# Kernel optimization log

Measured on AMD Instinct MI355X. Metric: run time of the kernel, lower is better.

The kernel has to match this reference:

```python
import jax, jax.numpy as jnp
import numpy as np
import math

EPS_LN = 1e-5
EPS_Q = 1e-5


def _layernorm(x):
    # LayerNorm without affine (elementwise_affine=False), biased variance
    mu = jnp.mean(x, axis=-1, keepdims=True)
    var = jnp.var(x, axis=-1, keepdims=True)
    return (x - mu) * jax.lax.rsqrt(var + EPS_LN)


def _quantize_activations(x):
    # per-row 8-bit absmax quantization
    eta = jnp.maximum(jnp.max(jnp.abs(x), axis=-1, keepdims=True), EPS_Q)
    x_q = jnp.clip(jnp.round(x * (127.0 / eta)), -128.0, 127.0)
    return x_q, eta / 127.0


def _quantize_weights(w):
    # absmean ternary quantization
    gamma = jnp.maximum(jnp.mean(jnp.abs(w)), EPS_Q)
    w_q = jnp.round(jnp.clip(w / gamma, -1.0, 1.0))
    return w_q, gamma


def setup_inputs() -> dict:
    key = jax.random.key(0)
    k1, k2 = jax.random.split(key, 2)
    B, S, IN, OUT = 2, 4096, 2048, 8192
    x = jax.random.normal(k1, (B, S, IN), dtype=jnp.float32)
    # kaiming_uniform_(a=sqrt(5)) -> U(-1/sqrt(fan_in), 1/sqrt(fan_in))
    bound = 1.0 / math.sqrt(IN)
    weight = jax.random.uniform(k2, (OUT, IN), dtype=jnp.float32, minval=-bound, maxval=bound)
    bias = jnp.zeros((OUT,), dtype=jnp.float32)
    return {"x": x, "weight": weight, "bias": bias}


def reference(x, weight, bias):
    x_norm = _layernorm(x)
    x_q, x_scale = _quantize_activations(x_norm)      # [B,S,K], [B,S,1]
    w_q, w_scale = _quantize_weights(weight)           # [N,K], scalar
    # int8 GEMM emulated exactly in fp32 (values are small integers, exact)
    out_i = jnp.einsum('bsk,nk->bsn', x_q, w_q)        # int32-equivalent accum
    out = out_i * (w_scale * x_scale) + bias
    return out
```

## Files before the change

kernel.cpp:

```cpp
#include <hip/hip_runtime.h>
#include <stdint.h>

typedef int v4i __attribute__((ext_vector_type(4)));

#define M_DIM 8192
#define N_DIM 8192
#define K_DIM 2048
#define RISKY_TAU 1e-4f
#define BUCKET_CAP 1024
#define SLOT 32768

#define ASYNC16(g, l) __builtin_amdgcn_global_load_lds(                        \
    (const __attribute__((address_space(1))) void*)(uintptr_t)(g),             \
    (__attribute__((address_space(3))) void*)(uint32_t)(uintptr_t)(l), 16, 0, 0)

__global__ __launch_bounds__(256) void abssum_stage1(const float* __restrict__ w,
                                                     float* __restrict__ s1) {
  int b = blockIdx.x * 256 + threadIdx.x;
  const float* p = w + (size_t)b * 128;
  float r[8];
#pragma unroll
  for (int j = 0; j < 8; j++) r[j] = fabsf(p[j]);
  for (int i = 8; i < 128; i += 8) {
#pragma unroll
    for (int j = 0; j < 8; j++) r[j] += fabsf(p[i + j]);
  }
  s1[b] = ((r[0] + r[1]) + (r[2] + r[3])) + ((r[4] + r[5]) + (r[6] + r[7]));
}

__global__ __launch_bounds__(256) void abssum_stage2(const float* __restrict__ s1,
                                                     float* __restrict__ s2) {
  int t = blockIdx.x * 256 + threadIdx.x;
  float v[32];
#pragma unroll
  for (int i = 0; i < 32; i++) v[i] = s1[t * 32 + i];
#pragma unroll
  for (int s = 1; s < 32; s *= 2) {
#pragma unroll
    for (int i = 0; i < 32; i += 2 * s) v[i] += v[i + s];
  }
  s2[t] = v[0];
}

__global__ __launch_bounds__(256) void gamma_stage3(const float* __restrict__ s2,
                                                    float* __restrict__ gp) {
  int t = threadIdx.x;
  float v[16];
#pragma unroll
  for (int i = 0; i < 16; i++) v[i] = s2[t * 16 + i];
#pragma unroll
  for (int s = 1; s < 16; s *= 2) {
#pragma unroll
    for (int i = 0; i < 16; i += 2 * s) v[i] += v[i + s];
  }
  __shared__ float sm[256];
  sm[t] = v[0];
  for (int s = 1; s < 256; s *= 2) {
    __syncthreads();
    if ((t & (2 * s - 1)) == 0) sm[t] += sm[t + s];
  }
  __syncthreads();
  if (t == 0) {
    float g = sm[0] * 0x1p-24f;
    gp[0] = fmaxf(g, 1e-5f);
  }
}

__global__ void zero_counts(int* __restrict__ counts) {
  counts[threadIdx.x] = 0;
}

__global__ __launch_bounds__(256) void wq_kernel(const float4* __restrict__ w4,
                                                 const float* __restrict__ gp,
                                                 int* __restrict__ wq,
                                                 int* __restrict__ counts,
                                                 int* __restrict__ buckets) {
  int i = blockIdx.x * 256 + threadIdx.x;
  float g = gp[0];
  float4 v = w4[i];
  float e[4] = {v.x, v.y, v.z, v.w};
  int q[4];
#pragma unroll
  for (int c = 0; c < 4; c++) {
    q[c] = (int)rintf(fminf(fmaxf(e[c] / g, -1.0f), 1.0f));
    float t = fabsf(e[c]) / g;
    if (fabsf(t - 0.5f) < RISKY_TAU) {
      int flat = i * 4 + c;
      int n = flat >> 11;
      int k = flat & 2047;
      int sgn_neg = (e[c] < 0.0f) ? 1 : 0;
      int sbit = (q[c] == 0) ? sgn_neg : (1 - sgn_neg);
      int b = n >> 7;
      int idx = atomicAdd(&counts[b], 1);
      if (idx < BUCKET_CAP)
        buckets[b * BUCKET_CAP + idx] = k | (n << 11) | (sbit << 24);
    }
  }
  wq[i] = (q[0] & 0xFF) | ((q[1] & 0xFF) << 8) | ((q[2] & 0xFF) << 16) | ((q[3] & 0xFF) << 24);
}

__global__ __launch_bounds__(256) void lnq_kernel(const float* __restrict__ x,
                                                  const float* __restrict__ gp,
                                                  int8_t* __restrict__ xq,
                                                  float* __restrict__ scales) {
  const int row = blockIdx.x;
  const int t = threadIdx.x;
  const float4* xr = (const float4*)(x + (size_t)row * K_DIM);
  float4 a = xr[t];
  float4 b = xr[t + 256];
  double v[8] = {a.x, a.y, a.z, a.w, b.x, b.y, b.z, b.w};
  double s = 0.0, ss = 0.0;
#pragma unroll
  for (int i = 0; i < 8; i++) { s += v[i]; ss += v[i] * v[i]; }
  __shared__ double sm1[256], sm2[256];
  sm1[t] = s; sm2[t] = ss;
  __syncthreads();
  for (int off = 128; off > 0; off >>= 1) {
    if (t < off) { sm1[t] += sm1[t + off]; sm2[t] += sm2[t + off]; }
    __syncthreads();
  }
  double mu = sm1[0] * (1.0 / 2048.0);
  double var = sm2[0] * (1.0 / 2048.0) - mu * mu;
  double inv = 1.0 / sqrt(var + 1e-5);
  __syncthreads();
  double mx = 0.0;
#pragma unroll
  for (int i = 0; i < 8; i++) {
    v[i] = (v[i] - mu) * inv;
    double av = fabs(v[i]);
    if (av > mx) mx = av;
  }
  sm1[t] = mx;
  __syncthreads();
  for (int off = 128; off > 0; off >>= 1) {
    if (t < off) sm1[t] = fmax(sm1[t], sm1[t + off]);
    __syncthreads();
  }
  double eta = fmax(sm1[0], 1e-5);
  double r = 127.0 / eta;
  int q[8];
#pragma unroll
  for (int i = 0; i < 8; i++) {
    double qq = rint(v[i] * r);
    qq = fmin(fmax(qq, -128.0), 127.0);
    q[i] = (int)qq;
  }
  int p0 = (q[0] & 0xFF) | ((q[1] & 0xFF) << 8) | ((q[2] & 0xFF) << 16) | ((q[3] & 0xFF) << 24);
  int p1 = (q[4] & 0xFF) | ((q[5] & 0xFF) << 8) | ((q[6] & 0xFF) << 16) | ((q[7] & 0xFF) << 24);
  int* orow = (int*)(xq + (size_t)row * K_DIM);
  orow[t] = p0;
  orow[t + 256] = p1;
  if (t == 0) scales[row] = (float)((double)gp[0] * eta * (1.0 / 127.0));
}

__global__ __launch_bounds__(512) void gemm_i8_kernel(const int8_t* __restrict__ A,
                                                      const int8_t* __restrict__ B,
                                                      const float* __restrict__ scales,
                                                      const float* __restrict__ bias,
                                                      const int* __restrict__ counts,
                                                      const int* __restrict__ buckets,
                                                      float* __restrict__ C) {
  __shared__ alignas(16) int8_t lds[3 * SLOT];
  const int tid = threadIdx.x;
  const int wave = tid >> 6;
  const int lane = tid & 63;

  const int b = blockIdx.x;
  const int tr = (b & 7) * 4 + ((b >> 3) & 3);
  const int tc = b >> 5;
  const int brow = tr * 256;
  const int bcol = tc * 256;

  const int chunkr = lane >> 2;
  const int sl = lane & 3;
  const int8_t* gA[2];
  const int8_t* gB[2];
  int dA[2], dB[2];
#pragma unroll
  for (int c = 0; c < 2; c++) {
    int ch = wave * 2 + c;
    int r = ch * 16 + chunkr;
    int scol = ((sl ^ ((r >> 1) & 3)) << 4);
    gA[c] = A + (size_t)(brow + r) * K_DIM + scol;
    gB[c] = B + (size_t)(bcol + r) * K_DIM + scol;
    dA[c] = ch * 1024;
    dB[c] = 16384 + ch * 1024;
  }

  const int wr = wave >> 2;
  const int wc = wave & 3;
  const int ks = lane >> 4;
  int aoff[8], boff[4];
#pragma unroll
  for (int m = 0; m < 8; m++) {
    int r = wr * 128 + m * 16 + (lane & 15);
    aoff[m] = r * 64 + ((ks ^ ((r >> 1) & 3)) << 4);
  }
#pragma unroll
  for (int n = 0; n < 4; n++) {
    int r = wc * 64 + n * 16 + (lane & 15);
    boff[n] = 16384 + r * 64 + ((ks ^ ((r >> 1) & 3)) << 4);
  }

  v4i acc[8][4];
  const v4i vzero = {0, 0, 0, 0};
#pragma unroll
  for (int m = 0; m < 8; m++)
#pragma unroll
    for (int n = 0; n < 4; n++) acc[m][n] = vzero;

#pragma unroll
  for (int c = 0; c < 2; c++) {
    ASYNC16(gA[c], lds + dA[c]);
    ASYNC16(gB[c], lds + dB[c]);
  }
#pragma unroll
  for (int c = 0; c < 2; c++) {
    ASYNC16(gA[c] + 64, lds + SLOT + dA[c]);
    ASYNC16(gB[c] + 64, lds + SLOT + dB[c]);
  }

  int rbase = 0;
  int sbase = 2 * SLOT;
  for (int t = 0; t < 32; ++t) {
    if (t < 31) asm volatile("s_waitcnt vmcnt(4)" ::: "memory");
    else        asm volatile("s_waitcnt vmcnt(0)" ::: "memory");
    __builtin_amdgcn_s_barrier();
    if (t < 30) {
      const int kt = (t + 2) * 64;
#pragma unroll
      for (int c = 0; c < 2; c++) {
        ASYNC16(gA[c] + kt, lds + sbase + dA[c]);
        ASYNC16(gB[c] + kt, lds + sbase + dB[c]);
      }
    }
    v4i bf[4], af[8];
#pragma unroll
    for (int n = 0; n < 4; n++) bf[n] = *(const v4i*)(lds + rbase + boff[n]);
#pragma unroll
    for (int m = 0; m < 8; m++) af[m] = *(const v4i*)(lds + rbase + aoff[m]);
    __builtin_amdgcn_s_setprio(1);
#pragma unroll
    for (int m = 0; m < 8; m++)
#pragma unroll
      for (int n = 0; n < 4; n++)
        acc[m][n] = __builtin_amdgcn_mfma_i32_16x16x64_i8(af[m], bf[n], acc[m][n], 0, 0, 0);
    __builtin_amdgcn_s_setprio(0);
    rbase = (rbase == 2 * SLOT) ? 0 : rbase + SLOT;
    sbase = (sbase == 2 * SLOT) ? 0 : sbase + SLOT;
  }

#pragma unroll
  for (int m = 0; m < 8; m++)
#pragma unroll
    for (int n = 0; n < 4; n++) acc[m][n] = acc[m][n] + acc[m][n];

  const int crow0 = brow + wr * 128;
  const int ccol0 = bcol + wc * 64;

#define CORR(J)                                                                \
  {                                                                            \
    _Pragma("unroll") for (int m = 0; m < 8; m++) {                            \
      _Pragma("unroll") for (int r = 0; r < 4; r++) {                          \
        int grow = crow0 + m * 16 + ((lane >> 4) << 2) + r;                    \
        int xv = (int)A[(size_t)grow * K_DIM + k];                             \
        acc[m][J][r] += sv * xv;                                               \
      }                                                                        \
    }                                                                          \
  }

  {
    int bkt = (bcol + wc * 64) >> 7;
    int cnt = counts[bkt];
    if (cnt > BUCKET_CAP) cnt = BUCKET_CAP;
    const int* bk = buckets + bkt * BUCKET_CAP;
    for (int e = 0; e < cnt; ++e) {
      int word = bk[e];
      int k = word & 2047;
      int nc = (word >> 11) & 8191;
      int sv = ((word >> 24) & 1) ? -1 : 1;
      if (((nc >> 6) & 1) == (wc & 1) && (nc & 15) == (lane & 15)) {
        int j = (nc >> 4) & 3;
        switch (j) {
          case 0: CORR(0); break;
          case 1: CORR(1); break;
          case 2: CORR(2); break;
          case 3: CORR(3); break;
        }
      }
    }
  }
#undef CORR

#pragma unroll
  for (int m = 0; m < 8; m++) {
#pragma unroll
    for (int r = 0; r < 4; r++) {
      int grow = crow0 + m * 16 + ((lane >> 4) << 2) + r;
      float sc = scales[grow] * 0.5f;
      float* crow = C + (size_t)grow * N_DIM;
#pragma unroll
      for (int n = 0; n < 4; n++) {
        int gcol = ccol0 + n * 16 + (lane & 15);
        crow[gcol] = (float)acc[m][n][r] * sc + bias[gcol];
      }
    }
  }
}

extern "C" void kernel_launch(void* const* d_in, const int* in_sizes, int n_in,
                              void* d_out, int out_size, void* d_ws, size_t ws_size,
                              hipStream_t stream) {
  const float* x = (const float*)d_in[0];
  const float* w = (const float*)d_in[1];
  const float* bias = (const float*)d_in[2];
  float* out = (float*)d_out;

  char* ws = (char*)d_ws;
  float* s1 = (float*)(ws);
  float* s2 = (float*)(ws + 0x100000);
  float* gamma_f = (float*)(ws + 0x110000);
  float* scales = (float*)(ws + 0x120000);
  int* counts = (int*)(ws + 0x130000);
  int* buckets = (int*)(ws + 0x131000);
  int8_t* Aq = (int8_t*)(ws + 0x200000);
  int8_t* Wq = (int8_t*)(ws + 0x200000 + (size_t)M_DIM * K_DIM);

  abssum_stage1<<<512, 256, 0, stream>>>(w, s1);
  abssum_stage2<<<16, 256, 0, stream>>>(s1, s2);
  gamma_stage3<<<1, 256, 0, stream>>>(s2, gamma_f);
  zero_counts<<<1, 64, 0, stream>>>(counts);
  wq_kernel<<<(N_DIM * K_DIM / 4 + 255) / 256, 256, 0, stream>>>(
      (const float4*)w, gamma_f, (int*)Wq, counts, buckets);
  lnq_kernel<<<M_DIM, 256, 0, stream>>>(x, gamma_f, Aq, scales);
  gemm_i8_kernel<<<1024, 512, 0, stream>>>(Aq, Wq, scales, bias, counts, buckets, out);
}
```

Measured before the change: 280.2 us.

## Interleave LDS reads and async global loads across four MFMA phases per K-tile

Measured after the change: 293.5 us. 4.7% more time.

```diff
diff --git a/kernel.cpp b/kernel.cpp
--- a/kernel.cpp
+++ b/kernel.cpp
@@ -219,36 +219,67 @@
     ASYNC16(gA[c] + 64, lds + SLOT + dA[c]);
     ASYNC16(gB[c] + 64, lds + SLOT + dB[c]);
   }
+  asm volatile("s_waitcnt vmcnt(4)" ::: "memory");
+  __builtin_amdgcn_s_barrier();
+
+#define MFMA2(M)                                                               \
+  _Pragma("unroll") for (int n = 0; n < 4; n++)                                \
+    acc[M][n] = __builtin_amdgcn_mfma_i32_16x16x64_i8(af[M], bf[n], acc[M][n], 0, 0, 0); \
+  _Pragma("unroll") for (int n = 0; n < 4; n++)                                \
+    acc[M + 1][n] = __builtin_amdgcn_mfma_i32_16x16x64_i8(af[M + 1], bf[n], acc[M + 1][n], 0, 0, 0);
 
   int rbase = 0;
   int sbase = 2 * SLOT;
   for (int t = 0; t < 32; ++t) {
-    if (t < 31) asm volatile("s_waitcnt vmcnt(4)" ::: "memory");
-    else        asm volatile("s_waitcnt vmcnt(0)" ::: "memory");
-    __builtin_amdgcn_s_barrier();
-    if (t < 30) {
-      const int kt = (t + 2) * 64;
-#pragma unroll
-      for (int c = 0; c < 2; c++) {
-        ASYNC16(gA[c] + kt, lds + sbase + dA[c]);
-        ASYNC16(gB[c] + kt, lds + sbase + dB[c]);
-      }
-    }
+    const int kt = (t + 2) * 64;
+    const bool st = (t < 30);
     v4i bf[4], af[8];
-#pragma unroll
-    for (int n = 0; n < 4; n++) bf[n] = *(const v4i*)(lds + rbase + boff[n]);
-#pragma unroll
-    for (int m = 0; m < 8; m++) af[m] = *(const v4i*)(lds + rbase + aoff[m]);
+    bf[0] = *(const v4i*)(lds + rbase + boff[0]);
+    bf[1] = *(const v4i*)(lds + rbase + boff[1]);
+    bf[2] = *(const v4i*)(lds + rbase + boff[2]);
+    bf[3] = *(const v4i*)(lds + rbase + boff[3]);
+    af[0] = *(const v4i*)(lds + rbase + aoff[0]);
+    af[1] = *(const v4i*)(lds + rbase + aoff[1]);
+    if (st) ASYNC16(gA[0] + kt, lds + sbase + dA[0]);
+    __builtin_amdgcn_s_barrier();
     __builtin_amdgcn_s_setprio(1);
-#pragma unroll
-    for (int m = 0; m < 8; m++)
-#pragma unroll
-      for (int n = 0; n < 4; n++)
-        acc[m][n] = __builtin_amdgcn_mfma_i32_16x16x64_i8(af[m], bf[n], acc[m][n], 0, 0, 0);
+    MFMA2(0)
     __builtin_amdgcn_s_setprio(0);
+    __builtin_amdgcn_s_barrier();
+    asm volatile("" ::: "memory");
+    af[2] = *(const v4i*)(lds + rbase + aoff[2]);
+    af[3] = *(const v4i*)(lds + rbase + aoff[3]);
+    if (st) ASYNC16(gA[1] + kt, lds + sbase + dA[1]);
+    __builtin_amdgcn_s_barrier();
+    __builtin_amdgcn_s_setprio(1);
+    MFMA2(2)
+    __builtin_amdgcn_s_setprio(0);
+    __builtin_amdgcn_s_barrier();
+    asm volatile("" ::: "memory");
+    af[4] = *(const v4i*)(lds + rbase + aoff[4]);
+    af[5] = *(const v4i*)(lds + rbase + aoff[5]);
+    if (st) ASYNC16(gB[0] + kt, lds + sbase + dB[0]);
+    __builtin_amdgcn_s_barrier();
+    __builtin_amdgcn_s_setprio(1);
+    MFMA2(4)
+    __builtin_amdgcn_s_setprio(0);
+    __builtin_amdgcn_s_barrier();
+    asm volatile("" ::: "memory");
+    af[6] = *(const v4i*)(lds + rbase + aoff[6]);
+    af[7] = *(const v4i*)(lds + rbase + aoff[7]);
+    if (st) ASYNC16(gB[1] + kt, lds + sbase + dB[1]);
+    if (t < 30)      asm volatile("s_waitcnt vmcnt(4)" ::: "memory");
+    else if (t == 30) asm volatile("s_waitcnt vmcnt(0)" ::: "memory");
+    __builtin_amdgcn_s_barrier();
+    __builtin_amdgcn_s_setprio(1);
+    MFMA2(6)
+    __builtin_amdgcn_s_setprio(0);
+    __builtin_amdgcn_s_barrier();
+    asm volatile("" ::: "memory");
     rbase = (rbase == 2 * SLOT) ? 0 : rbase + SLOT;
     sbase = (sbase == 2 * SLOT) ? 0 : sbase + SLOT;
   }
+#undef MFMA2
 
 #pragma unroll
   for (int m = 0; m < 8; m++)
```
